# Optimization experiments

Measured on AMD Instinct MI355X. Metric: run time of the kernel, lower is better.

## Reference

```python
import jax, jax.numpy as jnp
import numpy as np

BS, QLEN, DIM, H = 2, 2048, 2048, 16
DH = DIM // H


def setup_inputs() -> dict:
    key = jax.random.key(0)
    ks = jax.random.split(key, 10)
    s = 0.02
    return {
        "input": jax.random.normal(ks[0], (BS, QLEN, DIM), jnp.float32),
        "mask": jnp.ones((BS, QLEN), jnp.int32),
        "wq": jax.random.normal(ks[1], (DIM, DIM), jnp.float32) * s,
        "bq": jax.random.normal(ks[2], (DIM,), jnp.float32) * s,
        "wk": jax.random.normal(ks[3], (DIM, DIM), jnp.float32) * s,
        "bk": jax.random.normal(ks[4], (DIM,), jnp.float32) * s,
        "wv": jax.random.normal(ks[5], (DIM, DIM), jnp.float32) * s,
        "bv": jax.random.normal(ks[6], (DIM,), jnp.float32) * s,
        "wo": jax.random.normal(ks[7], (DIM, DIM), jnp.float32) * s,
        "bo": jax.random.normal(ks[8], (DIM,), jnp.float32) * s,
    }


def _shape(x, bs):
    # (bs, len, dim) -> (bs, H, len, DH)
    return x.reshape(bs, -1, H, DH).transpose(0, 2, 1, 3)


def reference(input, mask, wq, bq, wk, bk, wv, bv, wo, bo):
    bs, qlen, dim = input.shape
    # torch Linear: y = x @ W.T + b
    q = _shape(input @ wq.T + bq, bs)  # (bs,H,q,dh)
    k = _shape(input @ wk.T + bk, bs)  # (bs,H,k,dh)
    v = _shape(input @ wv.T + bv, bs)  # (bs,H,k,dh)
    q = q / jnp.sqrt(jnp.asarray(DH, q.dtype))
    scores = jnp.einsum("bhqd,bhkd->bhqk", q, k)
    # mask (bs, klen): positions where mask==0 are masked with -inf
    neg = (mask == 0)[:, None, None, :]  # (bs,1,1,klen)
    scores = jnp.where(neg, -jnp.inf, scores)
    weights = jax.nn.softmax(scores.astype(jnp.float32), axis=-1).astype(scores.dtype)
    # dropout p=0 (eval): identity
    context = jnp.einsum("bhqk,bhkd->bhqd", weights, v)
    context = context.transpose(0, 2, 1, 3).reshape(bs, qlen, dim)
    return context @ wo.T + bo
```

## Files before the change

### kernel.cpp

```cpp
#include <hip/hip_runtime.h>
#include <hip/hip_bf16.h>

#define BS 2
#define QLEN 2048
#define DIM 2048
#define H 16
#define DH 128
#define MTOT (BS*QLEN)

typedef __hip_bfloat16 bf16;
using f32x4 = __attribute__((ext_vector_type(4))) float;
using s16x8 = __attribute__((ext_vector_type(8))) short;

__device__ inline void gload_lds16(const bf16* g, bf16* l) {
    __builtin_amdgcn_global_load_lds(
        (const __attribute__((address_space(1))) void*)g,
        (__attribute__((address_space(3))) void*)l,
        16, 0, 0);
}

__global__ __launch_bounds__(256) void cast6(
    const float* __restrict__ x,
    const float* __restrict__ w0, const float* __restrict__ w1,
    const float* __restrict__ w2, const float* __restrict__ w3,
    bf16* xo, bf16* o0, bf16* o1, bf16* o2, bf16* o3, int n4)
{
    const float* in; bf16* out;
    switch (blockIdx.y) {
        case 0:  in = w0; out = o0; break;
        case 1:  in = w1; out = o1; break;
        case 2:  in = w2; out = o2; break;
        case 3:  in = w3; out = o3; break;
        case 4:  in = x;        out = xo;        break;
        default: in = x + 4*(size_t)n4; out = xo + 4*(size_t)n4; break;
    }
    int i = blockIdx.x * 256 + threadIdx.x;
    if (i < n4) {
        float4 v = ((const float4*)in)[i];
        __hip_bfloat162 p0 = __float22bfloat162_rn(make_float2(v.x, v.y));
        __hip_bfloat162 p1 = __float22bfloat162_rn(make_float2(v.z, v.w));
        ((__hip_bfloat162*)out)[2*i]   = p0;
        ((__hip_bfloat162*)out)[2*i+1] = p1;
    }
}

__global__ __launch_bounds__(256) void gemm_qkv(
    const bf16* __restrict__ A,
    const bf16* __restrict__ Wq, const bf16* __restrict__ Wk, const bf16* __restrict__ Wv,
    const float* __restrict__ bq, const float* __restrict__ bk, const float* __restrict__ bv,
    bf16* __restrict__ Qo, bf16* __restrict__ Ko, bf16* __restrict__ Vo,
    float qscale)
{
    __shared__ __align__(16) bf16 smem[128*136];
    bf16* As = smem;
    bf16* Bs = smem + 128*64;

    const int z = blockIdx.z;
    const bf16*  B    = (z == 0) ? Wq : (z == 1) ? Wk : Wv;
    const float* bias = (z == 0) ? bq : (z == 1) ? bk : bv;
    const float  scale = (z == 0) ? qscale : 1.0f;

    const int t = threadIdx.x;
    const int lane = t & 63, w = t >> 6;
    const int row16 = lane & 15, quad = lane >> 4;
    const int m0 = blockIdx.y * 128, n0 = blockIdx.x * 128;
    const int mo = (w >> 1) * 64, no = (w & 1) * 64;

    f32x4 acc[4][4];
    for (int i = 0; i < 4; i++)
        for (int j = 0; j < 4; j++)
            acc[i][j] = (f32x4){0.f, 0.f, 0.f, 0.f};

    for (int kt = 0; kt < DIM; kt += 64) {
        __syncthreads();
        #pragma unroll
        for (int i = 0; i < 4; i++) {
            int idx = i*256 + t;
            int row = idx >> 3, g = idx & 7;
            int src = g ^ (row & 7);
            gload_lds16(A + (size_t)(m0 + row) * DIM + kt + src*8, &As[idx*8]);
            gload_lds16(B + (size_t)(n0 + row) * DIM + kt + src*8, &Bs[idx*8]);
        }
        __syncthreads();

        #pragma unroll
        for (int kh = 0; kh < 2; kh++) {
            s16x8 af[4], bfr[4];
            #pragma unroll
            for (int mt = 0; mt < 4; mt++)
                af[mt] = *(const s16x8*)&As[(mo + mt*16 + row16)*64 + (((kh*4+quad) ^ (row16&7)))*8];
            #pragma unroll
            for (int nt = 0; nt < 4; nt++)
                bfr[nt] = *(const s16x8*)&Bs[(no + nt*16 + row16)*64 + (((kh*4+quad) ^ (row16&7)))*8];
            #pragma unroll
            for (int mt = 0; mt < 4; mt++)
                #pragma unroll
                for (int nt = 0; nt < 4; nt++)
                    acc[mt][nt] = __builtin_amdgcn_mfma_f32_16x16x32_bf16(
                        af[mt], bfr[nt], acc[mt][nt], 0, 0, 0);
        }
    }

    if (z < 2) {
        bf16* out = (z == 0) ? Qo : Ko;
        for (int mt = 0; mt < 4; mt++)
            for (int nt = 0; nt < 4; nt++) {
                int n = n0 + no + nt*16 + row16;
                float bv_ = bias[n];
                for (int r = 0; r < 4; r++) {
                    int m = m0 + mo + mt*16 + quad*4 + r;
                    out[(size_t)m * DIM + n] = __float2bfloat16((acc[mt][nt][r] + bv_) * scale);
                }
            }
    } else {
        __syncthreads();
        bf16* Ts = smem;
        for (int mt = 0; mt < 4; mt++)
            for (int nt = 0; nt < 4; nt++) {
                int nn = no + nt*16 + row16;
                float bv_ = bias[n0 + nn];
                for (int r = 0; r < 4; r++) {
                    int mm = mo + mt*16 + quad*4 + r;
                    Ts[nn*136 + mm] = __float2bfloat16(acc[mt][nt][r] + bv_);
                }
            }
        __syncthreads();
        const int b = m0 >> 11, q0b = m0 & 2047;
        for (int i = 0; i < 8; i++) {
            int chunk = t + i*256;
            int row = chunk >> 4;
            int c16 = chunk & 15;
            s16x8 val = *(const s16x8*)&Ts[row*136 + c16*8];
            *(s16x8*)(Vo + ((size_t)(b*DIM + n0 + row))*QLEN + q0b + c16*8) = val;
        }
    }
}

__global__ __launch_bounds__(256) void gemm_out(
    const bf16* __restrict__ A, const bf16* __restrict__ B,
    const float* __restrict__ bias, float* __restrict__ out)
{
    __shared__ __align__(16) bf16 As[128*64];
    __shared__ __align__(16) bf16 Bs[128*64];

    const int t = threadIdx.x;
    const int lane = t & 63, w = t >> 6;
    const int row16 = lane & 15, quad = lane >> 4;
    const int m0 = blockIdx.y * 128, n0 = blockIdx.x * 128;
    const int mo = (w >> 1) * 64, no = (w & 1) * 64;

    f32x4 acc[4][4];
    for (int i = 0; i < 4; i++)
        for (int j = 0; j < 4; j++)
            acc[i][j] = (f32x4){0.f, 0.f, 0.f, 0.f};

    for (int kt = 0; kt < DIM; kt += 64) {
        __syncthreads();
        #pragma unroll
        for (int i = 0; i < 4; i++) {
            int idx = i*256 + t;
            int row = idx >> 3, g = idx & 7;
            int src = g ^ (row & 7);
            gload_lds16(A + (size_t)(m0 + row) * DIM + kt + src*8, &As[idx*8]);
            gload_lds16(B + (size_t)(n0 + row) * DIM + kt + src*8, &Bs[idx*8]);
        }
        __syncthreads();

        #pragma unroll
        for (int kh = 0; kh < 2; kh++) {
            s16x8 af[4], bfr[4];
            #pragma unroll
            for (int mt = 0; mt < 4; mt++)
                af[mt] = *(const s16x8*)&As[(mo + mt*16 + row16)*64 + (((kh*4+quad) ^ (row16&7)))*8];
            #pragma unroll
            for (int nt = 0; nt < 4; nt++)
                bfr[nt] = *(const s16x8*)&Bs[(no + nt*16 + row16)*64 + (((kh*4+quad) ^ (row16&7)))*8];
            #pragma unroll
            for (int mt = 0; mt < 4; mt++)
                #pragma unroll
                for (int nt = 0; nt < 4; nt++)
                    acc[mt][nt] = __builtin_amdgcn_mfma_f32_16x16x32_bf16(
                        af[mt], bfr[nt], acc[mt][nt], 0, 0, 0);
        }
    }

    for (int mt = 0; mt < 4; mt++)
        for (int nt = 0; nt < 4; nt++) {
            int n = n0 + no + nt*16 + row16;
            float bv_ = bias[n];
            for (int r = 0; r < 4; r++) {
                int m = m0 + mo + mt*16 + quad*4 + r;
                out[(size_t)m * DIM + n] = acc[mt][nt][r] + bv_;
            }
        }
}

__global__ __launch_bounds__(256, 2) void attn(
    const bf16* __restrict__ Q, const bf16* __restrict__ Kb,
    const bf16* __restrict__ Vt, const int* __restrict__ mask,
    bf16* __restrict__ Ctx)
{
    __shared__ __align__(16) bf16 Ks[2][64*128];
    __shared__ __align__(16) bf16 Vs[128*64];
    __shared__ __align__(16) bf16 Pl[4][32*64];

    const int t = threadIdx.x, w = t >> 6, lane = t & 63;
    const int row16 = lane & 15, quad = lane >> 4;
    const int bh = blockIdx.y, b = bh >> 4, h = bh & 15;
    const int q0 = blockIdx.x * 128 + w * 32;

    s16x8 qf[2][4];
    for (int qs = 0; qs < 2; qs++) {
        const bf16* qp = Q + (size_t)(b*QLEN + q0 + qs*16 + row16) * DIM + h*DH;
        for (int ks = 0; ks < 4; ks++)
            qf[qs][ks] = *(const s16x8*)(qp + ks*32 + quad*8);
    }

    f32x4 o[2][8];
    for (int qs = 0; qs < 2; qs++)
        for (int i = 0; i < 8; i++) o[qs][i] = (f32x4){0.f, 0.f, 0.f, 0.f};
    float lsum[2][4] = {{0.f,0.f,0.f,0.f},{0.f,0.f,0.f,0.f}};
    const int* mrow = mask + b * QLEN;

    const bf16* Kbase = Kb + (size_t)b*QLEN*DIM + h*DH;
    const bf16* Vbase = Vt + ((size_t)b*DIM + h*DH) * QLEN;

    #pragma unroll
    for (int i = 0; i < 4; i++) {
        int idx = i*256 + t;
        int kr = idx >> 4, kc = idx & 15;
        int kg = kc ^ (kr & 15);
        gload_lds16(Kbase + (size_t)kr * DIM + kg*8, &Ks[0][idx*8]);
    }

    for (int it = 0; it < QLEN/64; it++) {
        const int kt = it * 64, buf = it & 1;
        __syncthreads();

        if (it + 1 < QLEN/64) {
            #pragma unroll
            for (int i = 0; i < 4; i++) {
                int idx = i*256 + t;
                int kr = idx >> 4, kc = idx & 15;
                int kg = kc ^ (kr & 15);
                gload_lds16(Kbase + (size_t)(kt + 64 + kr) * DIM + kg*8, &Ks[buf^1][idx*8]);
            }
        }
        #pragma unroll
        for (int i = 0; i < 4; i++) {
            int idx = i*256 + t;
            int vd = idx >> 3, vc = idx & 7;
            int vg = vc ^ (vd & 7);
            gload_lds16(Vbase + (size_t)vd * QLEN + kt + vg*8, &Vs[idx*8]);
        }

        float mval[4];
        #pragma unroll
        for (int nt = 0; nt < 4; nt++)
            mval[nt] = (mrow[kt + nt*16 + row16] != 0) ? -20.0f : -1e30f;

        f32x4 sc[2][4];
        for (int qs = 0; qs < 2; qs++)
            for (int nt = 0; nt < 4; nt++) sc[qs][nt] = (f32x4){0.f, 0.f, 0.f, 0.f};
        #pragma unroll
        for (int ks = 0; ks < 4; ks++) {
            #pragma unroll
            for (int nt = 0; nt < 4; nt++) {
                int rrow = nt*16 + row16;
                int c = (ks*4 + quad) ^ row16;
                s16x8 kf = *(const s16x8*)&Ks[buf][rrow*128 + c*8];
                sc[0][nt] = __builtin_amdgcn_mfma_f32_16x16x32_bf16(qf[0][ks], kf, sc[0][nt], 0, 0, 0);
                sc[1][nt] = __builtin_amdgcn_mfma_f32_16x16x32_bf16(qf[1][ks], kf, sc[1][nt], 0, 0, 0);
            }
        }

        #pragma unroll
        for (int qs = 0; qs < 2; qs++) {
            #pragma unroll
            for (int r = 0; r < 4; r++) {
                int prow = qs*16 + quad*4 + r;
                float ts = 0.f;
                #pragma unroll
                for (int nt = 0; nt < 4; nt++) {
                    float p = exp2f(sc[qs][nt][r] + mval[nt]);
                    ts += p;
                    int chunk = nt*2 + (row16 >> 3);
                    int slot = chunk ^ (prow & 7);
                    Pl[w][prow*64 + slot*8 + (row16 & 7)] = __float2bfloat16(p);
                }
                lsum[qs][r] += ts;
            }
        }

        __syncthreads();

        #pragma unroll
        for (int kc = 0; kc < 2; kc++) {
            int pslot0 = ((kc*4 + quad) ^ (row16 & 7));
            s16x8 pf0 = *(const s16x8*)&Pl[w][(0*16 + row16)*64 + pslot0*8];
            s16x8 pf1 = *(const s16x8*)&Pl[w][(1*16 + row16)*64 + pslot0*8];
            #pragma unroll
            for (int nt = 0; nt < 8; nt++) {
                int d = nt*16 + row16;
                int c = (kc*4 + quad) ^ (d & 7);
                s16x8 vf = *(const s16x8*)&Vs[d*64 + c*8];
                o[0][nt] = __builtin_amdgcn_mfma_f32_16x16x32_bf16(pf0, vf, o[0][nt], 0, 0, 0);
                o[1][nt] = __builtin_amdgcn_mfma_f32_16x16x32_bf16(pf1, vf, o[1][nt], 0, 0, 0);
            }
        }
    }

    for (int qs = 0; qs < 2; qs++) {
        float inv[4];
        for (int r = 0; r < 4; r++) {
            float ts = lsum[qs][r];
            ts += __shfl_xor(ts, 1);
            ts += __shfl_xor(ts, 2);
            ts += __shfl_xor(ts, 4);
            ts += __shfl_xor(ts, 8);
            inv[r] = 1.0f / ts;
        }
        for (int nt = 0; nt < 8; nt++)
            for (int r = 0; r < 4; r++) {
                float v = o[qs][nt][r] * inv[r];
                Ctx[(size_t)(b*QLEN + q0 + qs*16 + quad*4 + r) * DIM + h*DH + nt*16 + row16] =
                    __float2bfloat16(v);
            }
    }
}

extern "C" void kernel_launch(void* const* d_in, const int* in_sizes, int n_in,
                              void* d_out, int out_size, void* d_ws, size_t ws_size,
                              hipStream_t stream) {
    const float* x    = (const float*)d_in[0];
    const int*   mask = (const int*)d_in[1];
    const float* wq   = (const float*)d_in[2];
    const float* bq   = (const float*)d_in[3];
    const float* wk   = (const float*)d_in[4];
    const float* bk   = (const float*)d_in[5];
    const float* wv   = (const float*)d_in[6];
    const float* bv   = (const float*)d_in[7];
    const float* wo   = (const float*)d_in[8];
    const float* bo   = (const float*)d_in[9];

    char* ws = (char*)d_ws;
    const size_t MB = 1024 * 1024;
    bf16* Xb  = (bf16*)(ws);
    bf16* Qb  = (bf16*)(ws + 16*MB);
    bf16* Kb  = (bf16*)(ws + 32*MB);
    bf16* Vtb = (bf16*)(ws + 48*MB);
    bf16* Wqb = (bf16*)(ws + 64*MB);
    bf16* Wkb = (bf16*)(ws + 72*MB);
    bf16* Wvb = (bf16*)(ws + 80*MB);
    bf16* Wob = (bf16*)(ws + 88*MB);
    bf16* Ctx = Xb;

    int n4w = (DIM*DIM) / 4;
    cast6<<<dim3(n4w/256, 6), 256, 0, stream>>>(x, wq, wk, wv, wo,
                                                Xb, Wqb, Wkb, Wvb, Wob, n4w);

    const float qscale = 0.08838834764831845f * 1.4426950408889634f;
    gemm_qkv<<<dim3(DIM/128, MTOT/128, 3), 256, 0, stream>>>(
        Xb, Wqb, Wkb, Wvb, bq, bk, bv, Qb, Kb, Vtb, qscale);

    attn<<<dim3(QLEN/128, BS*H), 256, 0, stream>>>(Qb, Kb, Vtb, mask, Ctx);

    gemm_out<<<dim3(DIM/128, MTOT/128), 256, 0, stream>>>(Ctx, Wob, bo, (float*)d_out);
}
```

Measured before the change: 419.6 us.

## Triple-buffer GEMM loads with 256x128 tiles, 8 waves, and block swizzle

```diff
diff --git a/kernel.cpp b/kernel.cpp
--- a/kernel.cpp
+++ b/kernel.cpp
@@ -7,6 +7,11 @@
 #define H 16
 #define DH 128
 #define MTOT (BS*QLEN)
+
+#define BM 256
+#define BN 128
+#define BK 64
+#define NT (DIM/BK)
 
 typedef __hip_bfloat16 bf16;
 using f32x4 = __attribute__((ext_vector_type(4))) float;
@@ -44,16 +49,16 @@
     }
 }
 
-__global__ __launch_bounds__(256) void gemm_qkv(
+__global__ __launch_bounds__(512, 2) void gemm_qkv(
     const bf16* __restrict__ A,
     const bf16* __restrict__ Wq, const bf16* __restrict__ Wk, const bf16* __restrict__ Wv,
     const float* __restrict__ bq, const float* __restrict__ bk, const float* __restrict__ bv,
     bf16* __restrict__ Qo, bf16* __restrict__ Ko, bf16* __restrict__ Vo,
     float qscale)
 {
-    __shared__ __align__(16) bf16 smem[128*136];
-    bf16* As = smem;
-    bf16* Bs = smem + 128*64;
+    __shared__ __align__(16) bf16 smem[3*BM*BK + 3*BN*BK];
+    bf16* const SA = smem;
+    bf16* const SB = smem + 3*BM*BK;
 
     const int z = blockIdx.z;
     const bf16*  B    = (z == 0) ? Wq : (z == 1) ? Wk : Wv;
@@ -63,42 +68,83 @@
     const int t = threadIdx.x;
     const int lane = t & 63, w = t >> 6;
     const int row16 = lane & 15, quad = lane >> 4;
-    const int m0 = blockIdx.y * 128, n0 = blockIdx.x * 128;
+    const int sid = blockIdx.y * gridDim.x + blockIdx.x;
+    const int swz = (sid & 7) * 32 + (sid >> 3);
+    const int m0 = (swz >> 4) * BM, n0 = (swz & 15) * BN;
     const int mo = (w >> 1) * 64, no = (w & 1) * 64;
+
+    auto stageA = [&](int kt, int bufi) {
+        bf16* dst = SA + bufi * (BM*BK);
+        #pragma unroll
+        for (int i = 0; i < 4; i++) {
+            int idx = i*512 + t;
+            int row = idx >> 3, g = idx & 7;
+            int src = g ^ (row & 7);
+            gload_lds16(A + (size_t)(m0 + row) * DIM + kt + src*8, dst + idx*8);
+        }
+    };
+    auto stageB = [&](int kt, int bufi) {
+        bf16* dst = SB + bufi * (BN*BK);
+        #pragma unroll
+        for (int i = 0; i < 2; i++) {
+            int idx = i*512 + t;
+            int row = idx >> 3, g = idx & 7;
+            int src = g ^ (row & 7);
+            gload_lds16(B + (size_t)(n0 + row) * DIM + kt + src*8, dst + idx*8);
+        }
+    };
 
     f32x4 acc[4][4];
     for (int i = 0; i < 4; i++)
         for (int j = 0; j < 4; j++)
             acc[i][j] = (f32x4){0.f, 0.f, 0.f, 0.f};
 
-    for (int kt = 0; kt < DIM; kt += 64) {
-        __syncthreads();
-        #pragma unroll
-        for (int i = 0; i < 4; i++) {
-            int idx = i*256 + t;
-            int row = idx >> 3, g = idx & 7;
-            int src = g ^ (row & 7);
-            gload_lds16(A + (size_t)(m0 + row) * DIM + kt + src*8, &As[idx*8]);
-            gload_lds16(B + (size_t)(n0 + row) * DIM + kt + src*8, &Bs[idx*8]);
-        }
-        __syncthreads();
-
+    stageA(0,    0); stageB(0,    0);
+    stageA(BK,   1); stageB(BK,   1);
+    stageA(2*BK, 2); stageB(2*BK, 2);
+    asm volatile("s_waitcnt vmcnt(12)" ::: "memory");
+    __builtin_amdgcn_s_barrier();
+    asm volatile("" ::: "memory");
+
+    int buf = 0;
+    for (int it = 0; it < NT; ++it) {
+        const bf16* Asb = SA + buf * (BM*BK);
+        const bf16* Bsb = SB + buf * (BN*BK);
         #pragma unroll
         for (int kh = 0; kh < 2; kh++) {
             s16x8 af[4], bfr[4];
             #pragma unroll
             for (int mt = 0; mt < 4; mt++)
-                af[mt] = *(const s16x8*)&As[(mo + mt*16 + row16)*64 + (((kh*4+quad) ^ (row16&7)))*8];
+                af[mt] = *(const s16x8*)&Asb[(mo + mt*16 + row16)*BK + (((kh*4+quad) ^ (row16&7)))*8];
             #pragma unroll
             for (int nt = 0; nt < 4; nt++)
-                bfr[nt] = *(const s16x8*)&Bs[(no + nt*16 + row16)*64 + (((kh*4+quad) ^ (row16&7)))*8];
+                bfr[nt] = *(const s16x8*)&Bsb[(no + nt*16 + row16)*BK + (((kh*4+quad) ^ (row16&7)))*8];
+            __builtin_amdgcn_s_setprio(1);
             #pragma unroll
             for (int mt = 0; mt < 4; mt++)
                 #pragma unroll
                 for (int nt = 0; nt < 4; nt++)
                     acc[mt][nt] = __builtin_amdgcn_mfma_f32_16x16x32_bf16(
                         af[mt], bfr[nt], acc[mt][nt], 0, 0, 0);
-        }
+            __builtin_amdgcn_s_setprio(0);
+        }
+        if (it < NT-1) {
+            asm volatile("s_waitcnt lgkmcnt(0)" ::: "memory");
+            __builtin_amdgcn_s_barrier();
+            asm volatile("" ::: "memory");
+            if (it < NT-3) {
+                stageA((it+3)*BK, buf); stageB((it+3)*BK, buf);
+                asm volatile("s_waitcnt vmcnt(12)" ::: "memory");
+            } else if (it == NT-3) {
+                asm volatile("s_waitcnt vmcnt(6)" ::: "memory");
+            } else {
+                asm volatile("s_waitcnt vmcnt(0)" ::: "memory");
+            }
+            asm volatile("" ::: "memory");
+            __builtin_amdgcn_s_barrier();
+            asm volatile("" ::: "memory");
+        }
+        buf = (buf == 2) ? 0 : buf + 1;
     }
 
     if (z < 2) {
@@ -121,67 +167,110 @@
                 float bv_ = bias[n0 + nn];
                 for (int r = 0; r < 4; r++) {
                     int mm = mo + mt*16 + quad*4 + r;
-                    Ts[nn*136 + mm] = __float2bfloat16(acc[mt][nt][r] + bv_);
+                    Ts[nn*264 + mm] = __float2bfloat16(acc[mt][nt][r] + bv_);
                 }
             }
         __syncthreads();
         const int b = m0 >> 11, q0b = m0 & 2047;
+        #pragma unroll
         for (int i = 0; i < 8; i++) {
-            int chunk = t + i*256;
-            int row = chunk >> 4;
-            int c16 = chunk & 15;
-            s16x8 val = *(const s16x8*)&Ts[row*136 + c16*8];
-            *(s16x8*)(Vo + ((size_t)(b*DIM + n0 + row))*QLEN + q0b + c16*8) = val;
-        }
-    }
-}
-
-__global__ __launch_bounds__(256) void gemm_out(
+            int chunk = i*512 + t;
+            int row = chunk >> 5;
+            int c = chunk & 31;
+            s16x8 val = *(const s16x8*)&Ts[row*264 + c*8];
+            *(s16x8*)(Vo + ((size_t)(b*DIM + n0 + row))*QLEN + q0b + c*8) = val;
+        }
+    }
+}
+
+__global__ __launch_bounds__(512, 2) void gemm_out(
     const bf16* __restrict__ A, const bf16* __restrict__ B,
     const float* __restrict__ bias, float* __restrict__ out)
 {
-    __shared__ __align__(16) bf16 As[128*64];
-    __shared__ __align__(16) bf16 Bs[128*64];
+    __shared__ __align__(16) bf16 smem[3*BM*BK + 3*BN*BK];
+    bf16* const SA = smem;
+    bf16* const SB = smem + 3*BM*BK;
 
     const int t = threadIdx.x;
     const int lane = t & 63, w = t >> 6;
     const int row16 = lane & 15, quad = lane >> 4;
-    const int m0 = blockIdx.y * 128, n0 = blockIdx.x * 128;
+    const int sid = blockIdx.y * gridDim.x + blockIdx.x;
+    const int swz = (sid & 7) * 32 + (sid >> 3);
+    const int m0 = (swz >> 4) * BM, n0 = (swz & 15) * BN;
     const int mo = (w >> 1) * 64, no = (w & 1) * 64;
+
+    auto stageA = [&](int kt, int bufi) {
+        bf16* dst = SA + bufi * (BM*BK);
+        #pragma unroll
+        for (int i = 0; i < 4; i++) {
+            int idx = i*512 + t;
+            int row = idx >> 3, g = idx & 7;
+            int src = g ^ (row & 7);
+            gload_lds16(A + (size_t)(m0 + row) * DIM + kt + src*8, dst + idx*8);
+        }
+    };
+    auto stageB = [&](int kt, int bufi) {
+        bf16* dst = SB + bufi * (BN*BK);
+        #pragma unroll
+        for (int i = 0; i < 2; i++) {
+            int idx = i*512 + t;
+            int row = idx >> 3, g = idx & 7;
+            int src = g ^ (row & 7);
+            gload_lds16(B + (size_t)(n0 + row) * DIM + kt + src*8, dst + idx*8);
+        }
+    };
 
     f32x4 acc[4][4];
     for (int i = 0; i < 4; i++)
         for (int j = 0; j < 4; j++)
             acc[i][j] = (f32x4){0.f, 0.f, 0.f, 0.f};
 
-    for (int kt = 0; kt < DIM; kt += 64) {
-        __syncthreads();
-        #pragma unroll
-        for (int i = 0; i < 4; i++) {
-            int idx = i*256 + t;
-            int row = idx >> 3, g = idx & 7;
-            int src = g ^ (row & 7);
-            gload_lds16(A + (size_t)(m0 + row) * DIM + kt + src*8, &As[idx*8]);
-            gload_lds16(B + (size_t)(n0 + row) * DIM + kt + src*8, &Bs[idx*8]);
-        }
-        __syncthreads();
-
+    stageA(0,    0); stageB(0,    0);
+    stageA(BK,   1); stageB(BK,   1);
+    stageA(2*BK, 2); stageB(2*BK, 2);
+    asm volatile("s_waitcnt vmcnt(12)" ::: "memory");
+    __builtin_amdgcn_s_barrier();
+    asm volatile("" ::: "memory");
+
+    int buf = 0;
+    for (int it = 0; it < NT; ++it) {
+        const bf16* Asb = SA + buf * (BM*BK);
+        const bf16* Bsb = SB + buf * (BN*BK);
         #pragma unroll
         for (int kh = 0; kh < 2; kh++) {
             s16x8 af[4], bfr[4];
             #pragma unroll
             for (int mt = 0; mt < 4; mt++)
-                af[mt] = *(const s16x8*)&As[(mo + mt*16 + row16)*64 + (((kh*4+quad) ^ (row16&7)))*8];
+                af[mt] = *(const s16x8*)&Asb[(mo + mt*16 + row16)*BK + (((kh*4+quad) ^ (row16&7)))*8];
             #pragma unroll
             for (int nt = 0; nt < 4; nt++)
-                bfr[nt] = *(const s16x8*)&Bs[(no + nt*16 + row16)*64 + (((kh*4+quad) ^ (row16&7)))*8];
+                bfr[nt] = *(const s16x8*)&Bsb[(no + nt*16 + row16)*BK + (((kh*4+quad) ^ (row16&7)))*8];
+            __builtin_amdgcn_s_setprio(1);
             #pragma unroll
             for (int mt = 0; mt < 4; mt++)
                 #pragma unroll
                 for (int nt = 0; nt < 4; nt++)
                     acc[mt][nt] = __builtin_amdgcn_mfma_f32_16x16x32_bf16(
                         af[mt], bfr[nt], acc[mt][nt], 0, 0, 0);
-        }
+            __builtin_amdgcn_s_setprio(0);
+        }
+        if (it < NT-1) {
+            asm volatile("s_waitcnt lgkmcnt(0)" ::: "memory");
+            __builtin_amdgcn_s_barrier();
+            asm volatile("" ::: "memory");
+            if (it < NT-3) {
+                stageA((it+3)*BK, buf); stageB((it+3)*BK, buf);
+                asm volatile("s_waitcnt vmcnt(12)" ::: "memory");
+            } else if (it == NT-3) {
+                asm volatile("s_waitcnt vmcnt(6)" ::: "memory");
+            } else {
+                asm volatile("s_waitcnt vmcnt(0)" ::: "memory");
+            }
+            asm volatile("" ::: "memory");
+            __builtin_amdgcn_s_barrier();
+            asm volatile("" ::: "memory");
+        }
+        buf = (buf == 2) ? 0 : buf + 1;
     }
 
     for (int mt = 0; mt < 4; mt++)
@@ -206,8 +295,10 @@
 
     const int t = threadIdx.x, w = t >> 6, lane = t & 63;
     const int row16 = lane & 15, quad = lane >> 4;
-    const int bh = blockIdx.y, b = bh >> 4, h = bh & 15;
-    const int q0 = blockIdx.x * 128 + w * 32;
+    const int sid = blockIdx.y * gridDim.x + blockIdx.x;
+    const int swz = (sid & 7) * 64 + (sid >> 3);
+    const int bh = swz >> 4, b = bh >> 4, h = bh & 15;
+    const int q0 = (swz & 15) * 128 + w * 32;
 
     s16x8 qf[2][4];
     for (int qs = 0; qs < 2; qs++) {
@@ -360,10 +451,10 @@
                                                 Xb, Wqb, Wkb, Wvb, Wob, n4w);
 
     const float qscale = 0.08838834764831845f * 1.4426950408889634f;
-    gemm_qkv<<<dim3(DIM/128, MTOT/128, 3), 256, 0, stream>>>(
+    gemm_qkv<<<dim3(DIM/BN, MTOT/BM, 3), 512, 0, stream>>>(
         Xb, Wqb, Wkb, Wvb, bq, bk, bv, Qb, Kb, Vtb, qscale);
 
     attn<<<dim3(QLEN/128, BS*H), 256, 0, stream>>>(Qb, Kb, Vtb, mask, Ctx);
 
-    gemm_out<<<dim3(DIM/128, MTOT/128), 256, 0, stream>>>(Ctx, Wob, bo, (float*)d_out);
-}
+    gemm_out<<<dim3(DIM/BN, MTOT/BM), 512, 0, stream>>>(Ctx, Wob, bo, (float*)d_out);
+}
```

After: 400.1 us. 1.05x faster.
